# Optimization experiments

Measured on AMD Instinct MI355X. Metric: run time of the kernel, lower is better.

## Reference

```python
import jax, jax.numpy as jnp
import numpy as np
from jax import lax

B_SZ, SEQ, D_MODEL, D_STATE, DT_RANK = 4, 4096, 256, 16, 16


def setup_inputs() -> dict:
    key = jax.random.key(0)
    ks = jax.random.split(key, 12)
    d, n, r = D_MODEL, D_STATE, DT_RANK
    inp = {}
    inp["hidden_states"] = jax.random.normal(ks[0], (B_SZ, SEQ, d), jnp.float32)
    inp["in_proj_w"] = jax.random.normal(ks[1], (3 * d, d), jnp.float32) * (d ** -0.5)
    inp["x_proj_w"] = jax.random.normal(ks[2], (r + 2 * n, d), jnp.float32) * (d ** -0.5)
    s = r ** -0.5
    inp["dt_proj_w"] = jax.random.uniform(ks[3], (d, r), jnp.float32, -s, s)
    dt = jnp.exp(jax.random.uniform(ks[4], (d,), jnp.float32) * (np.log(0.1) - np.log(1e-3)) + np.log(1e-3))
    inp["dt_proj_b"] = dt + jnp.log(-jnp.expm1(-dt))  # inverse-softplus init
    inp["A_log"] = jnp.log(jnp.broadcast_to(jnp.arange(1, n + 1, dtype=jnp.float32), (d, n)))
    inp["D"] = jnp.ones((d,), jnp.float32)
    inp["out_proj1_w"] = jax.random.normal(ks[5], (d, d), jnp.float32) * (d ** -0.5)
    inp["conv_x_w"] = jax.random.normal(ks[6], (d, 1, 1), jnp.float32)
    inp["conv_x_b"] = jax.random.normal(ks[7], (d,), jnp.float32) * 0.1
    inp["conv_y_w"] = jax.random.normal(ks[8], (d, 1, 3), jnp.float32) * (3 ** -0.5)
    inp["conv_y_b"] = jax.random.normal(ks[9], (d,), jnp.float32) * 0.1
    inp["conv_z_w"] = jax.random.normal(ks[10], (d, 1, 5), jnp.float32) * (5 ** -0.5)
    inp["conv_z_b"] = jax.random.normal(ks[11], (d,), jnp.float32) * 0.1
    return inp


def _silu(x):
    return x * jax.nn.sigmoid(x)


def _dwconv(x, w, b):
    # x: (b, d, l); w: (d, 1, k) depthwise; 'same' padding (odd k)
    k = w.shape[-1]
    pad = (k - 1) // 2
    out = lax.conv_general_dilated(
        x, w, window_strides=(1,), padding=[(pad, pad)],
        dimension_numbers=("NCH", "OIH", "NCH"), feature_group_count=x.shape[1])
    return out + b[None, :, None]


def _selective_scan(u, delta, A, B, C, D, delta_bias):
    # u, delta: (b,d,l); A: (d,n); B,C: (b,n,l); D, delta_bias: (d,)
    delta = jax.nn.softplus(delta + delta_bias[None, :, None])
    dA = jnp.exp(jnp.einsum("bdl,dn->lbdn", delta, A))          # (l,b,d,n)
    dBu = jnp.einsum("bdl,bnl,bdl->lbdn", delta, B, u)           # (l,b,d,n)
    Ct = jnp.transpose(C, (2, 0, 1))                             # (l,b,n)

    def step(h, inp):
        dA_t, dBu_t, C_t = inp
        h = dA_t * h + dBu_t                                     # (b,d,n)
        y = jnp.einsum("bdn,bn->bd", h, C_t)
        return h, y

    h0 = jnp.zeros(u.shape[:2] + (A.shape[1],), u.dtype)
    _, ys = lax.scan(step, h0, (dA, dBu, Ct))                    # ys: (l,b,d)
    y = jnp.transpose(ys, (1, 2, 0))                             # (b,d,l)
    return y + D[None, :, None] * u


def reference(hidden_states, in_proj_w, x_proj_w, dt_proj_w, dt_proj_b, A_log, D,
              out_proj1_w, conv_x_w, conv_x_b, conv_y_w, conv_y_b, conv_z_w, conv_z_b):
    b, l, d = hidden_states.shape
    xyz = jnp.einsum("ble,de->bdl", hidden_states, in_proj_w)    # (b, 3d, l)
    x, y, z = jnp.split(xyz, 3, axis=1)                          # each (b,d,l)
    A = -jnp.exp(A_log.astype(jnp.float32))
    x = _silu(_dwconv(x, conv_x_w, conv_x_b))
    y = _silu(_dwconv(y, conv_y_w, conv_y_b))
    z = _silu(_dwconv(z, conv_z_w, conv_z_b))
    x_dbl = jnp.einsum("bdl,ed->ble", x, x_proj_w)               # (b,l,r+2n)
    dt_r, Bm, Cm = jnp.split(x_dbl, [DT_RANK, DT_RANK + D_STATE], axis=-1)
    # dt_proj applies bias here; selective_scan adds delta_bias again (faithful to source)
    dt = jnp.einsum("blr,dr->bdl", dt_r, dt_proj_w) + dt_proj_b[None, :, None]
    Bm = jnp.transpose(Bm, (0, 2, 1))                            # (b,n,l)
    Cm = jnp.transpose(Cm, (0, 2, 1))
    p = _selective_scan(x, dt, A, Bm, Cm, D.astype(jnp.float32), dt_proj_b.astype(jnp.float32))
    p = jnp.transpose(p, (0, 2, 1))                              # (b,l,d)
    y = jnp.transpose(y, (0, 2, 1))
    z = jnp.transpose(z, (0, 2, 1))
    l1 = jnp.einsum("bld,ed->ble", p * y, out_proj1_w)
    l2 = l1 * z
    l2 = _dwconv(jnp.transpose(l2, (0, 2, 1)), conv_x_w, conv_x_b)
    return jnp.transpose(l2, (0, 2, 1))                          # (b,l,d)
```

## Files before the change

kernel.cpp:

```cpp
#include <hip/hip_runtime.h>
#include <hip/hip_bf16.h>
#include <math.h>

typedef __hip_bfloat16 bf16;
typedef __attribute__((ext_vector_type(8))) short bf16x8;
typedef __attribute__((ext_vector_type(4))) float f32x4;

#define B_SZ 4
#define SEQ  4096
#define DM   256
#define NST  16
#define NCHK 64
#define LC   (SEQ/NCHK)
#define MT   (B_SZ*SEQ)
#define NLIN (B_SZ*16*256)

#define LOG2E 1.4426950408889634f

__device__ __forceinline__ float silu_f(float v){ return v / (1.f + __expf(-v)); }
__device__ __forceinline__ float softplus_f(float v){
  return (v > 15.f) ? v : __logf(1.f + __expf(v));
}
__device__ __forceinline__ short f2bf(float f){
  union { bf16 h; short s; } u; u.h = __float2bfloat16(f); return u.s;
}
__device__ __forceinline__ float bf2f(short s){
  union { unsigned int i; float f; } v;
  v.i = ((unsigned int)(unsigned short)s) << 16; return v.f;
}
__device__ __forceinline__ unsigned short f2h(float f){
  union { unsigned short u; _Float16 h; } v; v.h = (_Float16)f; return v.u;
}
__device__ __forceinline__ float h2f(unsigned short s){
  union { unsigned short u; _Float16 h; } v; v.u = s; return (float)v.h;
}
__device__ __forceinline__ short4 f4_to_bf4(float4 f){
  short4 s; s.x = f2bf(f.x); s.y = f2bf(f.y); s.z = f2bf(f.z); s.w = f2bf(f.w);
  return s;
}
__device__ __forceinline__ bf16x8 f8_to_bf8(float4 a, float4 b){
  bf16x8 v;
  v[0]=f2bf(a.x); v[1]=f2bf(a.y); v[2]=f2bf(a.z); v[3]=f2bf(a.w);
  v[4]=f2bf(b.x); v[5]=f2bf(b.y); v[6]=f2bf(b.z); v[7]=f2bf(b.w);
  return v;
}

__device__ __forceinline__ void async_cp16(const short* g, short* l){
  __builtin_amdgcn_global_load_lds(
      (const __attribute__((address_space(1))) unsigned int*)g,
      (__attribute__((address_space(3))) unsigned int*)l, 16, 0, 0);
}

template<int CTRL>
__device__ __forceinline__ float dpp_add_step(float v){
  int x = __builtin_amdgcn_update_dpp(0, __float_as_int(v), CTRL, 0xf, 0xf, true);
  return v + __int_as_float(x);
}

__global__ __launch_bounds__(256)
void cvt_w_k(const float* __restrict__ w_in, const float* __restrict__ w_o1,
             short* __restrict__ w_in_b, short* __restrict__ w_o1_b)
{
  int i = blockIdx.x * 256 + threadIdx.x;
  if (i < 49152) {
    float4 q = *(const float4*)&w_in[i * 4];
    *(short4*)&w_in_b[i * 4] = f4_to_bf4(q);
  } else {
    int j = i - 49152;
    float4 q = *(const float4*)&w_o1[j * 4];
    *(short4*)&w_o1_b[j * 4] = f4_to_bf4(q);
  }
}

__global__ __launch_bounds__(256)
void mfma_gemm_conv_k(const float* __restrict__ Av,
                      const short* __restrict__ Bw,
                      const float* __restrict__ wx, const float* __restrict__ bx,
                      const float* __restrict__ wy, const float* __restrict__ by,
                      const float* __restrict__ wz, const float* __restrict__ bz,
                      short* __restrict__ xout, short* __restrict__ yout,
                      short* __restrict__ zout)
{
  constexpr int RM = 80;
  __shared__ __align__(16) char smem_c[26624];
  short* As = (short*)smem_c;
  short* Bs = (short*)(smem_c + 10240);
  const int tid  = threadIdx.x;
  const int wave = tid >> 6, lane = tid & 63;
  const int quad = lane >> 4, l16 = lane & 15;
  const int wn = wave * 32;
  const int m0 = blockIdx.x * 64, n0 = blockIdx.y * 128;

  f32x4 acc[5][2] = {};

  for (int k0 = 0; k0 < 256; k0 += 64) {
    #pragma unroll
    for (int p = 0; p < 4; p++) {
      int id = p * 256 + tid;
      int row = id >> 3, slot = id & 7;
      int gch = slot ^ (row & 7);
      async_cp16(Bw + (size_t)(n0 + row) * 256 + k0 + gch * 8,
                 &Bs[row * 64 + slot * 8]);
    }
    #pragma unroll
    for (int p = 0; p < 3; p++) {
      int id = p * 256 + tid;
      if (id < RM * 8) {
        int row = id >> 3, slot = id & 7;
        int gch = slot ^ (row & 7);
        int gm = m0 - 8 + row;
        gm = gm < 0 ? 0 : (gm > MT - 1 ? MT - 1 : gm);
        const float* src = Av + (size_t)gm * 256 + k0 + gch * 8;
        float4 q0 = *(const float4*)src;
        float4 q1 = *(const float4*)(src + 4);
        *(bf16x8*)&As[row * 64 + slot * 8] = f8_to_bf8(q0, q1);
      }
    }
    __syncthreads();
    #pragma unroll
    for (int ks = 0; ks < 2; ks++) {
      bf16x8 fa[5], fb[2];
      int sa = (ks * 4 + quad) ^ (l16 & 7);
      #pragma unroll
      for (int i = 0; i < 5; i++)
        fa[i] = *(const bf16x8*)&As[(i * 16 + l16) * 64 + sa * 8];
      #pragma unroll
      for (int j = 0; j < 2; j++)
        fb[j] = *(const bf16x8*)&Bs[(wn + j * 16 + l16) * 64 + sa * 8];
      #pragma unroll
      for (int i = 0; i < 5; i++)
        #pragma unroll
        for (int j = 0; j < 2; j++)
          acc[i][j] = __builtin_amdgcn_mfma_f32_16x16x32_bf16(fa[i], fb[j], acc[i][j], 0, 0, 0);
    }
    __syncthreads();
  }

  short* Ts = (short*)smem_c;
  #pragma unroll
  for (int i = 0; i < 5; i++) {
    #pragma unroll
    for (int j = 0; j < 2; j++) {
      int col = wn + j * 16 + l16;
      int row = i * 16 + quad * 4;
      short4 v;
      v.x = f2bf(acc[i][j][0]); v.y = f2bf(acc[i][j][1]);
      v.z = f2bf(acc[i][j][2]); v.w = f2bf(acc[i][j][3]);
      *(short4*)&Ts[col * 84 + row] = v;
    }
  }
  __syncthreads();

  const int cp = tid & 63, rg = tid >> 6;
  const int lc0 = cp * 2;
  const int lr0 = rg * 16;
  const int lbase = (m0 & (SEQ - 1)) + lr0;
  float ta[24], tb[24];
  {
    const short* q0 = &Ts[lc0 * 84 + lr0 + 4];
    #pragma unroll
    for (int q = 0; q < 6; q++) {
      short4 a = *(const short4*)&q0[q * 4];
      short4 b = *(const short4*)&q0[84 + q * 4];
      ta[q*4+0] = bf2f(a.x); ta[q*4+1] = bf2f(a.y);
      ta[q*4+2] = bf2f(a.z); ta[q*4+3] = bf2f(a.w);
      tb[q*4+0] = bf2f(b.x); tb[q*4+1] = bf2f(b.y);
      tb[q*4+2] = bf2f(b.z); tb[q*4+3] = bf2f(b.w);
    }
  }
  const int type = n0 >> 8;
  const int gq = n0 + lc0 - type * 256;
  if (type == 0) {
    float w0 = wx[gq], w1 = wx[gq + 1];
    float b0 = bx[gq], b1 = bx[gq + 1];
    #pragma unroll
    for (int t = 0; t < 16; t++) {
      short2 o;
      o.x = f2bf(silu_f(fmaf(ta[t + 4], w0, b0)));
      o.y = f2bf(silu_f(fmaf(tb[t + 4], w1, b1)));
      *(short2*)&xout[(size_t)(m0 + lr0 + t) * 256 + gq] = o;
    }
  } else if (type == 1) {
    float w0[3], w1[3];
    #pragma unroll
    for (int j = 0; j < 3; j++) { w0[j] = wy[gq*3 + j]; w1[j] = wy[(gq+1)*3 + j]; }
    float b0 = by[gq], b1 = by[gq + 1];
    #pragma unroll
    for (int t = 0; t < 16; t++) {
      float a0 = b0, a1 = b1;
      #pragma unroll
      for (int j = 0; j < 3; j++) {
        int l = lbase + t + j - 1;
        bool ok = ((unsigned)l < SEQ);
        a0 = fmaf(ok ? ta[t + 3 + j] : 0.f, w0[j], a0);
        a1 = fmaf(ok ? tb[t + 3 + j] : 0.f, w1[j], a1);
      }
      short2 o; o.x = f2bf(silu_f(a0)); o.y = f2bf(silu_f(a1));
      *(short2*)&yout[(size_t)(m0 + lr0 + t) * 256 + gq] = o;
    }
  } else {
    float w0[5], w1[5];
    #pragma unroll
    for (int j = 0; j < 5; j++) { w0[j] = wz[gq*5 + j]; w1[j] = wz[(gq+1)*5 + j]; }
    float b0 = bz[gq], b1 = bz[gq + 1];
    #pragma unroll
    for (int t = 0; t < 16; t++) {
      float a0 = b0, a1 = b1;
      #pragma unroll
      for (int j = 0; j < 5; j++) {
        int l = lbase + t + j - 2;
        bool ok = ((unsigned)l < SEQ);
        a0 = fmaf(ok ? ta[t + 2 + j] : 0.f, w0[j], a0);
        a1 = fmaf(ok ? tb[t + 2 + j] : 0.f, w1[j], a1);
      }
      short2 o; o.x = f2bf(silu_f(a0)); o.y = f2bf(silu_f(a1));
      *(short2*)&zout[(size_t)(m0 + lr0 + t) * 256 + gq] = o;
    }
  }
}

template<int EPI, bool OBF, int BM>
__global__ __launch_bounds__(256)
void mfma_gemm_k(const short* __restrict__ Av, const short* __restrict__ Bw,
                 void* __restrict__ Outv, int N, int K,
                 const float* __restrict__ bias, const short* __restrict__ zc,
                 const float* __restrict__ cwx)
{
  constexpr int BN = 128, BK = 64;
  constexpr int JF = (BM == 64) ? 2 : 4;
  __shared__ short As[BM * BK];
  __shared__ short Bs[BN * BK];
  const int tid  = threadIdx.x;
  const int wave = tid >> 6, lane = tid & 63;
  const int quad = lane >> 4, l16 = lane & 15;
  const int wm = (BM == 64) ? 0 : (wave & 1) * 64;
  const int wn = (BM == 64) ? wave * 32 : (wave >> 1) * 64;
  const int m0 = blockIdx.x * BM, n0 = blockIdx.y * BN;

  f32x4 acc[4][JF] = {};

  for (int k0 = 0; k0 < K; k0 += BK) {
    #pragma unroll
    for (int p = 0; p < BM * 8 / 256; p++) {
      int id = p * 256 + tid;
      int row = id >> 3, slot = id & 7;
      int gch = slot ^ (row & 7);
      async_cp16(Av + (size_t)(m0 + row) * K + k0 + gch * 8,
                 &As[row * 64 + slot * 8]);
    }
    #pragma unroll
    for (int p = 0; p < 4; p++) {
      int id = p * 256 + tid;
      int row = id >> 3, slot = id & 7;
      int gch = slot ^ (row & 7);
      async_cp16(Bw + (size_t)(n0 + row) * K + k0 + gch * 8,
                 &Bs[row * 64 + slot * 8]);
    }
    __syncthreads();
    #pragma unroll
    for (int ks = 0; ks < 2; ks++) {
      bf16x8 fa[4], fb[JF];
      int sa = (ks * 4 + quad) ^ (l16 & 7);
      #pragma unroll
      for (int i = 0; i < 4; i++)
        fa[i] = *(const bf16x8*)&As[(wm + i * 16 + l16) * 64 + sa * 8];
      #pragma unroll
      for (int j = 0; j < JF; j++)
        fb[j] = *(const bf16x8*)&Bs[(wn + j * 16 + l16) * 64 + sa * 8];
      #pragma unroll
      for (int i = 0; i < 4; i++)
        #pragma unroll
        for (int j = 0; j < JF; j++)
          acc[i][j] = __builtin_amdgcn_mfma_f32_16x16x32_bf16(fa[i], fb[j], acc[i][j], 0, 0, 0);
    }
    __syncthreads();
  }

  #pragma unroll
  for (int i = 0; i < 4; i++) {
    #pragma unroll
    for (int j = 0; j < JF; j++) {
      int n = n0 + wn + j * 16 + l16;
      #pragma unroll
      for (int r = 0; r < 4; r++) {
        int m = m0 + wm + i * 16 + quad * 4 + r;
        float v = acc[i][j][r];
        if constexpr (EPI == 2)
          v = v * bf2f(zc[(size_t)m * N + n]) * cwx[n] + bias[n];
        if constexpr (OBF) ((short*)Outv)[(size_t)m * N + n] = f2bf(v);
        else               ((float*)Outv)[(size_t)m * N + n] = v;
      }
    }
  }
}

__global__ __launch_bounds__(256)
void gemm34_k(const short* __restrict__ xcb,
              const float* __restrict__ Bw,
              const float* __restrict__ wdt,
              const float* __restrict__ bdt,
              float* __restrict__ xdbl,
              unsigned short* __restrict__ dtvh)
{
  constexpr int TM = 32, TK = 16, NN = 48;
  __shared__ __align__(16) float As[TK][TM + 4];
  __shared__ __align__(16) float Bs[TK][64 + 4];
  __shared__ __align__(16) float dt_s[TM][20];
  __shared__ __align__(16) float wdt_s[256][20];
  const int tid = threadIdx.x;
  const int tn = tid & 15, tm = tid >> 4;
  const int m0 = blockIdx.x * TM;
  float acc[2][4] = {};
  const int mlA = tid >> 3, kdA = (tid & 7) * 2;
  const int mlB = tid >> 2, kqB = (tid & 3) * 4;

  {
    float4 q0 = *(const float4*)&wdt[tid * 16 + 0];
    float4 q1 = *(const float4*)&wdt[tid * 16 + 4];
    float4 q2 = *(const float4*)&wdt[tid * 16 + 8];
    float4 q3 = *(const float4*)&wdt[tid * 16 + 12];
    *(float4*)&wdt_s[tid][0]  = q0;
    *(float4*)&wdt_s[tid][4]  = q1;
    *(float4*)&wdt_s[tid][8]  = q2;
    *(float4*)&wdt_s[tid][12] = q3;
  }

  for (int k0 = 0; k0 < 256; k0 += TK) {
    {
      size_t off = (size_t)(m0 + mlA) * 256 + k0 + kdA;
      unsigned int v = *(const unsigned int*)(xcb + off);
      As[kdA + 0][mlA] = bf2f((short)(v & 0xffffu));
      As[kdA + 1][mlA] = bf2f((short)(v >> 16));
    }
    {
      float v0 = 0.f, v1 = 0.f, v2 = 0.f, v3 = 0.f;
      if (mlB < NN) {
        float4 q = *(const float4*)(Bw + (size_t)mlB * 256 + k0 + kqB);
        v0 = q.x; v1 = q.y; v2 = q.z; v3 = q.w;
      }
      Bs[kqB+0][mlB] = v0; Bs[kqB+1][mlB] = v1; Bs[kqB+2][mlB] = v2; Bs[kqB+3][mlB] = v3;
    }
    __syncthreads();
    #pragma unroll
    for (int k = 0; k < TK; k++) {
      float2 av = *(const float2*)&As[k][tm << 1];
      float4 bv = *(const float4*)&Bs[k][tn << 2];
      float a[2] = {av.x, av.y};
      float b[4] = {bv.x, bv.y, bv.z, bv.w};
      #pragma unroll
      for (int i = 0; i < 2; i++)
        #pragma unroll
        for (int j = 0; j < 4; j++)
          acc[i][j] = fmaf(a[i], b[j], acc[i][j]);
    }
    __syncthreads();
  }

  #pragma unroll
  for (int i = 0; i < 2; i++) {
    int m = m0 + (tm << 1) + i;
    #pragma unroll
    for (int j = 0; j < 4; j++) {
      int n = (tn << 2) + j;
      float v = acc[i][j];
      if (n < NN) xdbl[(size_t)m * NN + n] = v;
      if (tn < 4) dt_s[(tm << 1) + i][n] = v;
    }
  }
  __syncthreads();

  const int c0 = tid & 63, rg = tid >> 6;
  float w[4][16];
  float bb[4];
  #pragma unroll
  for (int cc = 0; cc < 4; cc++) {
    int col = cc * 64 + c0;
    #pragma unroll
    for (int q = 0; q < 4; q++) {
      float4 t = *(const float4*)&wdt_s[col][q * 4];
      w[cc][q*4+0] = t.x; w[cc][q*4+1] = t.y; w[cc][q*4+2] = t.z; w[cc][q*4+3] = t.w;
    }
    bb[cc] = 2.f * bdt[col];
  }
  #pragma unroll
  for (int rr = 0; rr < 8; rr++) {
    int row = rg * 8 + rr;
    float dr[16];
    #pragma unroll
    for (int q = 0; q < 4; q++) {
      float4 t = *(const float4*)&dt_s[row][q * 4];
      dr[q*4+0] = t.x; dr[q*4+1] = t.y; dr[q*4+2] = t.z; dr[q*4+3] = t.w;
    }
    #pragma unroll
    for (int cc = 0; cc < 4; cc++) {
      float s = bb[cc];
      #pragma unroll
      for (int k = 0; k < 16; k++) s = fmaf(dr[k], w[cc][k], s);
      dtvh[(size_t)(m0 + row) * 256 + cc * 64 + c0] = f2h(softplus_f(s));
    }
  }
}

template<bool PASSC>
__global__ __launch_bounds__(256)
void scan_k(const short* __restrict__ xcb,
            const unsigned short* __restrict__ dtvh,
            const float* __restrict__ xdbl,
            const float* __restrict__ A_log,
            const float* __restrict__ Dp,
            const float* __restrict__ Hstart,
            float* __restrict__ Sdt, float* __restrict__ hfbuf,
            const short* __restrict__ ycb,
            short* __restrict__ poutb)
{
  __shared__ __align__(16) float2 du2_s[16 * 66];
  __shared__ __align__(16) float2 BC_s [PASSC ? 16 * 66 : 2];
  __shared__ __align__(16) float  Bc_s [PASSC ? 4 : 16 * 68];
  __shared__ __align__(16) float  y_s  [PASSC ? 16 * 68 : 4];
  const int tid = threadIdx.x;
  const int n = tid & 15, dl = tid >> 4;
  const int ch = blockIdx.x;
  const int d0 = blockIdx.y * 16;
  const int b  = blockIdx.z;
  const int d  = d0 + dl;
  const int t0 = ch * LC;
  const size_t brow = (size_t)b * SEQ;
  const size_t cidx = (size_t)ch * NLIN + ((size_t)b * 16 + blockIdx.y) * 256 + tid;

  {
    const int tq = tid >> 2;
    const int dq = (tid & 3) * 4;
    size_t row = brow + t0 + tq;
    ushort4 xv = *(const ushort4*)(xcb + row * 256 + d0 + dq);
    ushort4 dv = *(const ushort4*)(dtvh + row * 256 + d0 + dq);
    float dt0 = h2f(dv.x), dt1 = h2f(dv.y), dt2 = h2f(dv.z), dt3 = h2f(dv.w);
    du2_s[(dq + 0) * 66 + tq] = make_float2(dt0, dt0 * bf2f((short)xv.x));
    du2_s[(dq + 1) * 66 + tq] = make_float2(dt1, dt1 * bf2f((short)xv.y));
    du2_s[(dq + 2) * 66 + tq] = make_float2(dt2, dt2 * bf2f((short)xv.z));
    du2_s[(dq + 3) * 66 + tq] = make_float2(dt3, dt3 * bf2f((short)xv.w));
    if constexpr (PASSC) {
      float4 Bq = *(const float4*)(xdbl + row * 48 + 16 + dq);
      float4 Cq = *(const float4*)(xdbl + row * 48 + 32 + dq);
      BC_s[(dq + 0) * 66 + tq] = make_float2(Bq.x, Cq.x);
      BC_s[(dq + 1) * 66 + tq] = make_float2(Bq.y, Cq.y);
      BC_s[(dq + 2) * 66 + tq] = make_float2(Bq.z, Cq.z);
      BC_s[(dq + 3) * 66 + tq] = make_float2(Bq.w, Cq.w);
    } else {
      float4 Bq = *(const float4*)(xdbl + row * 48 + 16 + dq);
      Bc_s[(dq + 0) * 68 + tq] = Bq.x;
      Bc_s[(dq + 1) * 68 + tq] = Bq.y;
      Bc_s[(dq + 2) * 68 + tq] = Bq.z;
      Bc_s[(dq + 3) * 68 + tq] = Bq.w;
    }
  }
  float u_r[4];
  if constexpr (PASSC) {
    #pragma unroll
    for (int i = 0; i < 4; i++) {
      int t = (tid >> 4) + i * 16;
      u_r[i] = bf2f(xcb[(brow + t0 + t) * 256 + d0 + n]);
    }
  }
  __syncthreads();

  const float A2 = -__expf(A_log[d * NST + n]) * LOG2E;

  float h = PASSC ? Hstart[cidx] : 0.f;
  float sdt = 0.f;
  for (int t4 = 0; t4 < LC; t4 += 4) {
    float4 a = *(const float4*)&du2_s[dl * 66 + t4];
    float4 c = *(const float4*)&du2_s[dl * 66 + t4 + 2];
    float dA[4], du[4];
    dA[0] = __builtin_amdgcn_exp2f(a.x * A2); du[0] = a.y;
    dA[1] = __builtin_amdgcn_exp2f(a.z * A2); du[1] = a.w;
    dA[2] = __builtin_amdgcn_exp2f(c.x * A2); du[2] = c.y;
    dA[3] = __builtin_amdgcn_exp2f(c.z * A2); du[3] = c.w;
    if constexpr (!PASSC) {
      sdt += (a.x + a.z) + (c.x + c.z);
      float4 f = *(const float4*)&Bc_s[n * 68 + t4];
      float Bv[4] = {f.x, f.y, f.z, f.w};
      #pragma unroll
      for (int j = 0; j < 4; j++)
        h = fmaf(dA[j], h, du[j] * Bv[j]);
    } else {
      float4 e = *(const float4*)&BC_s[n * 66 + t4];
      float4 g = *(const float4*)&BC_s[n * 66 + t4 + 2];
      float Bv[4] = {e.x, e.z, g.x, g.z};
      float Cv[4] = {e.y, e.w, g.y, g.w};
      float yv[4];
      #pragma unroll
      for (int j = 0; j < 4; j++) {
        h = fmaf(dA[j], h, du[j] * Bv[j]);
        yv[j] = h * Cv[j];
      }
      #pragma unroll
      for (int j = 0; j < 4; j++) yv[j] = dpp_add_step<0x118>(yv[j]);
      #pragma unroll
      for (int j = 0; j < 4; j++) yv[j] = dpp_add_step<0x114>(yv[j]);
      #pragma unroll
      for (int j = 0; j < 4; j++) yv[j] = dpp_add_step<0x112>(yv[j]);
      #pragma unroll
      for (int j = 0; j < 4; j++) yv[j] = dpp_add_step<0x111>(yv[j]);
      if (n == 15)
        *(float4*)&y_s[dl * 68 + t4] = make_float4(yv[0], yv[1], yv[2], yv[3]);
    }
  }

  if constexpr (!PASSC) {
    hfbuf[cidx] = h;
    if (n == 0)
      Sdt[((size_t)ch * B_SZ + b) * 256 + d] = sdt;
  } else {
    __syncthreads();
    const float Dval = Dp[d0 + n];
    #pragma unroll
    for (int i = 0; i < 4; i++) {
      int t = (tid >> 4) + i * 16;
      size_t row = brow + t0 + t;
      float p = fmaf(Dval, u_r[i], y_s[n * 68 + t]);
      float yg = bf2f(ycb[row * 256 + d0 + n]);
      poutb[row * 256 + d0 + n] = f2bf(p * yg);
    }
  }
}

__global__ __launch_bounds__(64)
void scan_mid_k(const float* __restrict__ Sdt, const float* __restrict__ hfbuf,
                const float* __restrict__ A_log, float* __restrict__ Hstart)
{
  int lin = blockIdx.x * 64 + threadIdx.x;
  int b = lin >> 12;
  int d = (lin >> 4) & 255;
  int n = lin & 15;
  const float A2 = -__expf(A_log[d * NST + n]) * LOG2E;
  float H = 0.f;
  for (int c = 0; c < NCHK; c++) {
    size_t idx = (size_t)c * NLIN + lin;
    Hstart[idx] = H;
    float P = __builtin_amdgcn_exp2f(A2 * Sdt[((size_t)c * B_SZ + b) * 256 + d]);
    H = P * H + hfbuf[idx];
  }
}

extern "C" void kernel_launch(void* const* d_in, const int* in_sizes, int n_in,
                              void* d_out, int out_size, void* d_ws, size_t ws_size,
                              hipStream_t stream)
{
  const float* hs    = (const float*)d_in[0];
  const float* w_in  = (const float*)d_in[1];
  const float* w_xp  = (const float*)d_in[2];
  const float* w_dt  = (const float*)d_in[3];
  const float* b_dt  = (const float*)d_in[4];
  const float* A_log = (const float*)d_in[5];
  const float* Dp    = (const float*)d_in[6];
  const float* w_o1  = (const float*)d_in[7];
  const float* cwx   = (const float*)d_in[8];
  const float* cbx   = (const float*)d_in[9];
  const float* cwy   = (const float*)d_in[10];
  const float* cby   = (const float*)d_in[11];
  const float* cwz   = (const float*)d_in[12];
  const float* cbz   = (const float*)d_in[13];

  char* wsb = (char*)d_ws;
  short* xcb  = (short*)wsb;
  short* ycb  = xcb + (size_t)MT * 256;
  short* zcb  = ycb + (size_t)MT * 256;
  short* pbufb= zcb + (size_t)MT * 256;
  short* w_in_b = pbufb + (size_t)MT * 256;
  short* w_o1_b = w_in_b + 768 * 256;
  float* xdbl = (float*)(w_o1_b + 256 * 256 + 128);
  unsigned short* dtvh = (unsigned short*)(xdbl + (size_t)MT * 48);
  float* Sdtb = (float*)(dtvh + (size_t)MT * 256);
  float* hf   = Sdtb + (size_t)NCHK * B_SZ * 256;
  float* Hs   = hf   + (size_t)NCHK * NLIN;

  dim3 blk(256);

  cvt_w_k<<<dim3(256), blk, 0, stream>>>(w_in, w_o1, w_in_b, w_o1_b);

  mfma_gemm_conv_k<<<dim3(MT / 64, 768 / 128), blk, 0, stream>>>(
      hs, w_in_b, cwx, cbx, cwy, cby, cwz, cbz, xcb, ycb, zcb);

  gemm34_k<<<dim3(MT / 32), blk, 0, stream>>>(
      xcb, w_xp, w_dt, b_dt, xdbl, dtvh);

  scan_k<false><<<dim3(NCHK, DM / 16, B_SZ), blk, 0, stream>>>(
      xcb, dtvh, xdbl, A_log, Dp, nullptr, Sdtb, hf, nullptr, nullptr);
  scan_mid_k<<<dim3(NLIN / 64), dim3(64), 0, stream>>>(Sdtb, hf, A_log, Hs);
  scan_k<true><<<dim3(NCHK, DM / 16, B_SZ), blk, 0, stream>>>(
      xcb, dtvh, xdbl, A_log, Dp, Hs, nullptr, nullptr, ycb, pbufb);

  mfma_gemm_k<2, false, 64><<<dim3(MT / 64, 256 / 128), blk, 0, stream>>>(
      pbufb, w_o1_b, d_out, 256, 256, cbx, zcb, cwx);
}
```

Baseline: 192.3 us.

## Split second scan pass into dedicated kernel with four states per thread

The templated scan kernel is split in two. The chunk-summary pass is unchanged. The output pass becomes a new 64-thread-block kernel where each thread carries four state elements and does a partial C-dot in registers, needing only two DPP reduction steps instead of four. This cuts shuffle work and loads tiles row-wise with vectorized stores. The trade-off is fewer threads per block and less parallelism, with four serial exp2 chains per thread.

```diff
diff --git a/kernel.cpp b/kernel.cpp
--- a/kernel.cpp
+++ b/kernel.cpp
@@ -401,22 +401,15 @@
   }
 }
 
-template<bool PASSC>
 __global__ __launch_bounds__(256)
-void scan_k(const short* __restrict__ xcb,
-            const unsigned short* __restrict__ dtvh,
-            const float* __restrict__ xdbl,
-            const float* __restrict__ A_log,
-            const float* __restrict__ Dp,
-            const float* __restrict__ Hstart,
-            float* __restrict__ Sdt, float* __restrict__ hfbuf,
-            const short* __restrict__ ycb,
-            short* __restrict__ poutb)
+void scan_a_k(const short* __restrict__ xcb,
+              const unsigned short* __restrict__ dtvh,
+              const float* __restrict__ xdbl,
+              const float* __restrict__ A_log,
+              float* __restrict__ Sdt, float* __restrict__ hfbuf)
 {
   __shared__ __align__(16) float2 du2_s[16 * 66];
-  __shared__ __align__(16) float2 BC_s [PASSC ? 16 * 66 : 2];
-  __shared__ __align__(16) float  Bc_s [PASSC ? 4 : 16 * 68];
-  __shared__ __align__(16) float  y_s  [PASSC ? 16 * 68 : 4];
+  __shared__ __align__(16) float  Bc_s [16 * 68];
   const int tid = threadIdx.x;
   const int n = tid & 15, dl = tid >> 4;
   const int ch = blockIdx.x;
@@ -438,34 +431,17 @@
     du2_s[(dq + 1) * 66 + tq] = make_float2(dt1, dt1 * bf2f((short)xv.y));
     du2_s[(dq + 2) * 66 + tq] = make_float2(dt2, dt2 * bf2f((short)xv.z));
     du2_s[(dq + 3) * 66 + tq] = make_float2(dt3, dt3 * bf2f((short)xv.w));
-    if constexpr (PASSC) {
-      float4 Bq = *(const float4*)(xdbl + row * 48 + 16 + dq);
-      float4 Cq = *(const float4*)(xdbl + row * 48 + 32 + dq);
-      BC_s[(dq + 0) * 66 + tq] = make_float2(Bq.x, Cq.x);
-      BC_s[(dq + 1) * 66 + tq] = make_float2(Bq.y, Cq.y);
-      BC_s[(dq + 2) * 66 + tq] = make_float2(Bq.z, Cq.z);
-      BC_s[(dq + 3) * 66 + tq] = make_float2(Bq.w, Cq.w);
-    } else {
-      float4 Bq = *(const float4*)(xdbl + row * 48 + 16 + dq);
-      Bc_s[(dq + 0) * 68 + tq] = Bq.x;
-      Bc_s[(dq + 1) * 68 + tq] = Bq.y;
-      Bc_s[(dq + 2) * 68 + tq] = Bq.z;
-      Bc_s[(dq + 3) * 68 + tq] = Bq.w;
-    }
-  }
-  float u_r[4];
-  if constexpr (PASSC) {
-    #pragma unroll
-    for (int i = 0; i < 4; i++) {
-      int t = (tid >> 4) + i * 16;
-      u_r[i] = bf2f(xcb[(brow + t0 + t) * 256 + d0 + n]);
-    }
+    float4 Bq = *(const float4*)(xdbl + row * 48 + 16 + dq);
+    Bc_s[(dq + 0) * 68 + tq] = Bq.x;
+    Bc_s[(dq + 1) * 68 + tq] = Bq.y;
+    Bc_s[(dq + 2) * 68 + tq] = Bq.z;
+    Bc_s[(dq + 3) * 68 + tq] = Bq.w;
   }
   __syncthreads();
 
   const float A2 = -__expf(A_log[d * NST + n]) * LOG2E;
 
-  float h = PASSC ? Hstart[cidx] : 0.f;
+  float h = 0.f;
   float sdt = 0.f;
   for (int t4 = 0; t4 < LC; t4 += 4) {
     float4 a = *(const float4*)&du2_s[dl * 66 + t4];
@@ -475,53 +451,17 @@
     dA[1] = __builtin_amdgcn_exp2f(a.z * A2); du[1] = a.w;
     dA[2] = __builtin_amdgcn_exp2f(c.x * A2); du[2] = c.y;
     dA[3] = __builtin_amdgcn_exp2f(c.z * A2); du[3] = c.w;
-    if constexpr (!PASSC) {
-      sdt += (a.x + a.z) + (c.x + c.z);
-      float4 f = *(const float4*)&Bc_s[n * 68 + t4];
-      float Bv[4] = {f.x, f.y, f.z, f.w};
-      #pragma unroll
-      for (int j = 0; j < 4; j++)
-        h = fmaf(dA[j], h, du[j] * Bv[j]);
-    } else {
-      float4 e = *(const float4*)&BC_s[n * 66 + t4];
-      float4 g = *(const float4*)&BC_s[n * 66 + t4 + 2];
-      float Bv[4] = {e.x, e.z, g.x, g.z};
-      float Cv[4] = {e.y, e.w, g.y, g.w};
-      float yv[4];
-      #pragma unroll
-      for (int j = 0; j < 4; j++) {
-        h = fmaf(dA[j], h, du[j] * Bv[j]);
-        yv[j] = h * Cv[j];
-      }
-      #pragma unroll
-      for (int j = 0; j < 4; j++) yv[j] = dpp_add_step<0x118>(yv[j]);
-      #pragma unroll
-      for (int j = 0; j < 4; j++) yv[j] = dpp_add_step<0x114>(yv[j]);
-      #pragma unroll
-      for (int j = 0; j < 4; j++) yv[j] = dpp_add_step<0x112>(yv[j]);
-      #pragma unroll
-      for (int j = 0; j < 4; j++) yv[j] = dpp_add_step<0x111>(yv[j]);
-      if (n == 15)
-        *(float4*)&y_s[dl * 68 + t4] = make_float4(yv[0], yv[1], yv[2], yv[3]);
-    }
-  }
-
-  if constexpr (!PASSC) {
-    hfbuf[cidx] = h;
-    if (n == 0)
-      Sdt[((size_t)ch * B_SZ + b) * 256 + d] = sdt;
-  } else {
-    __syncthreads();
-    const float Dval = Dp[d0 + n];
-    #pragma unroll
-    for (int i = 0; i < 4; i++) {
-      int t = (tid >> 4) + i * 16;
-      size_t row = brow + t0 + t;
-      float p = fmaf(Dval, u_r[i], y_s[n * 68 + t]);
-      float yg = bf2f(ycb[row * 256 + d0 + n]);
-      poutb[row * 256 + d0 + n] = f2bf(p * yg);
-    }
-  }
+    sdt += (a.x + a.z) + (c.x + c.z);
+    float4 f = *(const float4*)&Bc_s[n * 68 + t4];
+    float Bv[4] = {f.x, f.y, f.z, f.w};
+    #pragma unroll
+    for (int j = 0; j < 4; j++)
+      h = fmaf(dA[j], h, du[j] * Bv[j]);
+  }
+
+  hfbuf[cidx] = h;
+  if (n == 0)
+    Sdt[((size_t)ch * B_SZ + b) * 256 + d] = sdt;
 }
 
 __global__ __launch_bounds__(64)
@@ -539,6 +479,117 @@
     Hstart[idx] = H;
     float P = __builtin_amdgcn_exp2f(A2 * Sdt[((size_t)c * B_SZ + b) * 256 + d]);
     H = P * H + hfbuf[idx];
+  }
+}
+
+__global__ __launch_bounds__(64)
+void scan_c_k(const short* __restrict__ xcb,
+              const unsigned short* __restrict__ dtvh,
+              const float* __restrict__ xdbl,
+              const float* __restrict__ A_log,
+              const float* __restrict__ Dp,
+              const float* __restrict__ Hstart,
+              const short* __restrict__ ycb,
+              short* __restrict__ poutb)
+{
+  __shared__ __align__(16) float2 du2_s[16 * 66];
+  __shared__ __align__(16) float2 BC_s [64 * 18];
+  __shared__ __align__(16) float  y_s  [16 * 68];
+  const int tid = threadIdx.x;
+  const int ch = blockIdx.x;
+  const int d0 = blockIdx.y * 16;
+  const int b  = blockIdx.z;
+  const int t0 = ch * LC;
+  const size_t brow = (size_t)b * SEQ;
+
+  {
+    const int r = tid;
+    size_t row = brow + t0 + r;
+    #pragma unroll
+    for (int q = 0; q < 4; q++) {
+      ushort4 xv = *(const ushort4*)(xcb + row * 256 + d0 + q * 4);
+      ushort4 dv = *(const ushort4*)(dtvh + row * 256 + d0 + q * 4);
+      float dt0 = h2f(dv.x), dt1 = h2f(dv.y), dt2 = h2f(dv.z), dt3 = h2f(dv.w);
+      du2_s[(q*4 + 0) * 66 + r] = make_float2(dt0, dt0 * bf2f((short)xv.x));
+      du2_s[(q*4 + 1) * 66 + r] = make_float2(dt1, dt1 * bf2f((short)xv.y));
+      du2_s[(q*4 + 2) * 66 + r] = make_float2(dt2, dt2 * bf2f((short)xv.z));
+      du2_s[(q*4 + 3) * 66 + r] = make_float2(dt3, dt3 * bf2f((short)xv.w));
+    }
+    #pragma unroll
+    for (int q = 0; q < 4; q++) {
+      float4 Bq = *(const float4*)(xdbl + row * 48 + 16 + q * 4);
+      float4 Cq = *(const float4*)(xdbl + row * 48 + 32 + q * 4);
+      *(float4*)&BC_s[r * 18 + q * 4 + 0] = make_float4(Bq.x, Cq.x, Bq.y, Cq.y);
+      *(float4*)&BC_s[r * 18 + q * 4 + 2] = make_float4(Bq.z, Cq.z, Bq.w, Cq.w);
+    }
+  }
+  __syncthreads();
+
+  const int dl = tid >> 2, nq = tid & 3;
+  const int d  = d0 + dl;
+
+  float A2[4], h[4];
+  #pragma unroll
+  for (int j = 0; j < 4; j++)
+    A2[j] = -__expf(A_log[d * NST + nq * 4 + j]) * LOG2E;
+  {
+    const size_t cb = (size_t)ch * NLIN +
+                      ((size_t)b * 16 + blockIdx.y) * 256 + dl * 16 + nq * 4;
+    float4 H = *(const float4*)(Hstart + cb);
+    h[0] = H.x; h[1] = H.y; h[2] = H.z; h[3] = H.w;
+  }
+
+  for (int t4 = 0; t4 < LC; t4 += 4) {
+    float4 a = *(const float4*)&du2_s[dl * 66 + t4];
+    float4 c = *(const float4*)&du2_s[dl * 66 + t4 + 2];
+    float dts[4] = {a.x, a.z, c.x, c.z};
+    float dus[4] = {a.y, a.w, c.y, c.w};
+    float yv[4];
+    #pragma unroll
+    for (int tt = 0; tt < 4; tt++) {
+      float4 e = *(const float4*)&BC_s[(t4 + tt) * 18 + nq * 4];
+      float4 g = *(const float4*)&BC_s[(t4 + tt) * 18 + nq * 4 + 2];
+      float dA0 = __builtin_amdgcn_exp2f(dts[tt] * A2[0]);
+      float dA1 = __builtin_amdgcn_exp2f(dts[tt] * A2[1]);
+      float dA2 = __builtin_amdgcn_exp2f(dts[tt] * A2[2]);
+      float dA3 = __builtin_amdgcn_exp2f(dts[tt] * A2[3]);
+      h[0] = fmaf(dA0, h[0], dus[tt] * e.x);
+      h[1] = fmaf(dA1, h[1], dus[tt] * e.z);
+      h[2] = fmaf(dA2, h[2], dus[tt] * g.x);
+      h[3] = fmaf(dA3, h[3], dus[tt] * g.z);
+      float s = h[0] * e.y;
+      s = fmaf(h[1], e.w, s);
+      s = fmaf(h[2], g.y, s);
+      s = fmaf(h[3], g.w, s);
+      yv[tt] = s;
+    }
+    #pragma unroll
+    for (int j = 0; j < 4; j++) yv[j] = dpp_add_step<0x112>(yv[j]);
+    #pragma unroll
+    for (int j = 0; j < 4; j++) yv[j] = dpp_add_step<0x111>(yv[j]);
+    if (nq == 3)
+      *(float4*)&y_s[dl * 68 + t4] = make_float4(yv[0], yv[1], yv[2], yv[3]);
+  }
+  __syncthreads();
+
+  {
+    const int r = tid;
+    size_t row = brow + t0 + r;
+    #pragma unroll
+    for (int q = 0; q < 4; q++) {
+      ushort4 xv = *(const ushort4*)(xcb + row * 256 + d0 + q * 4);
+      ushort4 yg = *(const ushort4*)(ycb + row * 256 + d0 + q * 4);
+      short4 o;
+      float p0 = fmaf(Dp[d0 + q*4 + 0], bf2f((short)xv.x), y_s[(q*4 + 0) * 68 + r]);
+      float p1 = fmaf(Dp[d0 + q*4 + 1], bf2f((short)xv.y), y_s[(q*4 + 1) * 68 + r]);
+      float p2 = fmaf(Dp[d0 + q*4 + 2], bf2f((short)xv.z), y_s[(q*4 + 2) * 68 + r]);
+      float p3 = fmaf(Dp[d0 + q*4 + 3], bf2f((short)xv.w), y_s[(q*4 + 3) * 68 + r]);
+      o.x = f2bf(p0 * bf2f((short)yg.x));
+      o.y = f2bf(p1 * bf2f((short)yg.y));
+      o.z = f2bf(p2 * bf2f((short)yg.z));
+      o.w = f2bf(p3 * bf2f((short)yg.w));
+      *(short4*)&poutb[row * 256 + d0 + q * 4] = o;
+    }
   }
 }
 
@@ -584,11 +635,11 @@
   gemm34_k<<<dim3(MT / 32), blk, 0, stream>>>(
       xcb, w_xp, w_dt, b_dt, xdbl, dtvh);
 
-  scan_k<false><<<dim3(NCHK, DM / 16, B_SZ), blk, 0, stream>>>(
-      xcb, dtvh, xdbl, A_log, Dp, nullptr, Sdtb, hf, nullptr, nullptr);
+  scan_a_k<<<dim3(NCHK, DM / 16, B_SZ), blk, 0, stream>>>(
+      xcb, dtvh, xdbl, A_log, Sdtb, hf);
   scan_mid_k<<<dim3(NLIN / 64), dim3(64), 0, stream>>>(Sdtb, hf, A_log, Hs);
-  scan_k<true><<<dim3(NCHK, DM / 16, B_SZ), blk, 0, stream>>>(
-      xcb, dtvh, xdbl, A_log, Dp, Hs, nullptr, nullptr, ycb, pbufb);
+  scan_c_k<<<dim3(NCHK, DM / 16, B_SZ), dim3(64), 0, stream>>>(
+      xcb, dtvh, xdbl, A_log, Dp, Hs, ycb, pbufb);
 
   mfma_gemm_k<2, false, 64><<<dim3(MT / 64, 256 / 128), blk, 0, stream>>>(
       pbufb, w_o1_b, d_out, 256, 256, cbx, zcb, cwx);
```

After: 197.3 us. 2.6% more time.
